# Kernel optimization log

Measured on AMD Instinct MI355X. Metric: run time of the kernel, lower is better.

Reference implementation:

```python
import jax, jax.numpy as jnp
import numpy as np

B, S, H = 32, 255, 1024
BS, WD, O = 120, 20, 10
HSZ = 2 * (BS + 1) + WD  # 262


def setup_inputs() -> dict:
    key = jax.random.key(0)
    ks = jax.random.split(key, 9)
    inv = lambda *d: 1.0 / np.sqrt(d[0])
    return {
        "state": jax.random.normal(ks[0], (B, S, H), jnp.float32),
        "head_w": jax.random.normal(ks[1], (H, BS), jnp.float32) * inv(H),
        "head_b": jax.random.normal(ks[2], (BS,), jnp.float32) * 0.02,
        "tail_w": jax.random.normal(ks[3], (H, BS), jnp.float32) * inv(H),
        "tail_b": jax.random.normal(ks[4], (BS,), jnp.float32) * 0.02,
        "U": jax.random.normal(ks[5], (O, BS, BS), jnp.float32) * inv(BS),
        "width_table": jax.random.normal(ks[6], (256, WD), jnp.float32).at[0].set(0.0),  # padding_idx=0
        "cls_w": jax.random.normal(ks[7], (O, HSZ), jnp.float32) * inv(HSZ),
        "cls_b": jax.random.normal(ks[8], (O,), jnp.float32) * 0.02,
    }


def _leaky_relu(x):
    return jnp.where(x >= 0, x, 0.01 * x)  # torch LeakyReLU default slope


def reference(state, head_w, head_b, tail_w, tail_b, U, width_table, cls_w, cls_b):
    b, s, _ = state.shape
    bs = head_w.shape[1]
    # head/tail MLPs (dropout is identity in eval)
    h = _leaky_relu(state @ head_w + head_b)  # (b, s, bs)
    t = _leaky_relu(state @ tail_w + tail_b)  # (b, s, bs)

    # bilinear term
    scores1 = jnp.einsum('bxi,oij,byj->bxyo', h, U, t)  # (b, s, s, O)

    # append bias-ones feature
    ones = jnp.ones((b, s, 1), h.dtype)
    h1 = jnp.concatenate([h, ones], axis=-1)  # (b, s, bs+1)
    t1 = jnp.concatenate([t, ones], axis=-1)

    # span-width embedding: pos[x, y] = y - x + 1, clamped to 0 for y < x
    pos = jnp.arange(s)[None, :] - jnp.arange(s)[:, None] + 1
    pos = pos * (pos > 0)
    wemb = width_table[pos]  # (s, s, WD)

    # cls(concat(h1_x, t1_y, wemb_xy)) decomposed into three small projections
    # + broadcast-add; mathematically identical to materializing affined_cat.
    Wh = cls_w[:, :bs + 1]              # (O, bs+1)
    Wt = cls_w[:, bs + 1:2 * (bs + 1)]  # (O, bs+1)
    Ww = cls_w[:, 2 * (bs + 1):]        # (O, WD)
    scores2 = (jnp.einsum('bxi,oi->bxo', h1, Wh)[:, :, None, :]
               + jnp.einsum('byi,oi->byo', t1, Wt)[:, None, :, :]
               + jnp.einsum('xyw,ow->xyo', wemb, Ww)[None]
               + cls_b)
    return scores1 + scores2
```

## Files before the change

### kernel.cpp

```cpp
#include <hip/hip_runtime.h>
#include <hip/hip_bf16.h>

using f32x4 = __attribute__((ext_vector_type(4))) float;
using s16x8 = __attribute__((ext_vector_type(8))) short;
using s16x4 = __attribute__((ext_vector_type(4))) short;

constexpr int RTOT = 32 * 255;

__device__ inline unsigned short f2bf(float x) {
    __hip_bfloat16 b = __float2bfloat16(x);
    return __builtin_bit_cast(unsigned short, b);
}
__device__ inline float bf2f(unsigned short u) {
    unsigned int t = ((unsigned int)u) << 16;
    return __builtin_bit_cast(float, t);
}
__device__ inline f32x4 mfma16(s16x8 a, s16x8 b, f32x4 c) {
    return __builtin_amdgcn_mfma_f32_16x16x32_bf16(a, b, c, 0, 0, 0);
}
__device__ inline void gload16(const unsigned short* g, unsigned short* l) {
    __builtin_amdgcn_global_load_lds(
        (const __attribute__((address_space(1))) void*)g,
        (__attribute__((address_space(3))) void*)l, 16, 0, 0);
}


__global__ __launch_bounds__(256) void convert_k(
    const float* __restrict__ head_w, const float* __restrict__ tail_w,
    const float* __restrict__ U, const float* __restrict__ wtab,
    const float* __restrict__ cls_w,
    unsigned short* __restrict__ WP, unsigned short* __restrict__ Ut,
    float* __restrict__ tblp)
{
    int gid = blockIdx.x * 256 + threadIdx.x;
    if (gid < 262144) {
        int e = gid & 7, kcp = (gid >> 3) & 7, n = (gid >> 6) & 255, ks = gid >> 14;
        int kc = kcp ^ (n & 7);
        int k = ks * 64 + kc * 8 + e;
        float v;
        if (n < 128) v = (n < 120) ? head_w[k * 120 + n] : 0.f;
        else { int nn = n - 128; v = (nn < 120) ? tail_w[k * 120 + nn] : 0.f; }
        WP[gid] = f2bf(v);
    } else if (gid < 262144 + 163840) {
        int idx = gid - 262144;
        int j = idx & 127, i2 = (idx >> 7) & 127, o = idx >> 14;
        float v = (i2 < 120 && j < 120) ? U[((size_t)o * 120 + i2) * 120 + j] : 0.f;
        Ut[(size_t)o * 16384 + (size_t)j * 128 + i2] = f2bf(v);
    } else {
        int id = gid - 262144 - 163840;
        if (id < 2560) {
            int p = id / 10, o = id - (id / 10) * 10;
            float s = 0.f;
            #pragma unroll
            for (int wq = 0; wq < 20; ++wq)
                s += wtab[p * 20 + wq] * cls_w[o * 262 + 242 + wq];
            tblp[p * 12 + o] = s;
        }
    }
}

__global__ __launch_bounds__(256) void ht_mfma(
    const float* __restrict__ state, const unsigned short* __restrict__ WP,
    const unsigned short* __restrict__ Ut,
    const float* __restrict__ head_b, const float* __restrict__ tail_b,
    const float* __restrict__ cls_w, const float* __restrict__ cls_b,
    unsigned short* __restrict__ tbuf, unsigned short* __restrict__ hUb,
    float* __restrict__ hwp, float* __restrict__ twp)
{
    __shared__ unsigned short Ss[2][32 * 64];
    __shared__ unsigned short Ws[2][256 * 64];
    const int r0 = blockIdx.x * 32;
    const int tid = threadIdx.x;
    const int w = tid >> 6, lane = tid & 63;
    const int l16 = lane & 15, kq = lane >> 4;
    const int srow = tid >> 3, skc = tid & 7;
    const float* sp = &state[(size_t)(r0 + srow) * 1024 + skc * 8];

    f32x4 acc[4][2];
    #pragma unroll
    for (int fn = 0; fn < 4; ++fn)
        #pragma unroll
        for (int fr = 0; fr < 2; ++fr) acc[fn][fr] = (f32x4){0.f, 0.f, 0.f, 0.f};

    #pragma unroll
    for (int j = 0; j < 8; ++j) {
        int off = (w * 8 + j) * 512;
        gload16(WP + off + lane * 8, &Ws[0][off]);
    }
    {
        f32x4 a0 = *(const f32x4*)sp;
        f32x4 a1 = *(const f32x4*)(sp + 4);
        s16x8 pk;
        #pragma unroll
        for (int e = 0; e < 4; ++e) { pk[e] = (short)f2bf(a0[e]); pk[e + 4] = (short)f2bf(a1[e]); }
        *(s16x8*)((char*)&Ss[0][0] + srow * 128 + ((skc * 16) ^ ((srow & 7) << 4))) = pk;
    }
    __syncthreads();

    for (int it = 0; it < 16; ++it) {
        const int cur = it & 1;
        f32x4 a0, a1;
        if (it < 15) {
            #pragma unroll
            for (int j = 0; j < 8; ++j) {
                int off = (w * 8 + j) * 512;
                gload16(WP + (it + 1) * 16384 + off + lane * 8, &Ws[cur ^ 1][off]);
            }
            a0 = *(const f32x4*)(sp + (it + 1) * 64);
            a1 = *(const f32x4*)(sp + (it + 1) * 64 + 4);
        }
        const char* SsB = (const char*)&Ss[cur][0];
        const char* WsB = (const char*)&Ws[cur][0];
        s16x8 bf[2][2];
        #pragma unroll
        for (int fr = 0; fr < 2; ++fr) {
            int rr = fr * 16 + l16;
            #pragma unroll
            for (int ks = 0; ks < 2; ++ks)
                bf[fr][ks] = *(const s16x8*)(SsB + rr * 128 + ((ks * 64 + kq * 16) ^ ((rr & 7) << 4)));
        }
        #pragma unroll
        for (int fn = 0; fn < 4; ++fn) {
            int n = w * 64 + fn * 16 + l16;
            #pragma unroll
            for (int ks = 0; ks < 2; ++ks) {
                s16x8 af = *(const s16x8*)(WsB + n * 128 + ((ks * 64 + kq * 16) ^ ((n & 7) << 4)));
                #pragma unroll
                for (int fr = 0; fr < 2; ++fr)
                    acc[fn][fr] = mfma16(af, bf[fr][ks], acc[fn][fr]);
            }
        }
        if (it < 15) {
            s16x8 pk;
            #pragma unroll
            for (int e = 0; e < 4; ++e) { pk[e] = (short)f2bf(a0[e]); pk[e + 4] = (short)f2bf(a1[e]); }
            *(s16x8*)((char*)&Ss[cur ^ 1][0] + srow * 128 + ((skc * 16) ^ ((srow & 7) << 4))) = pk;
        }
        __syncthreads();
    }

    unsigned short* Hl = &Ws[0][0];
    unsigned short* Tl = &Ws[1][0];
    #pragma unroll
    for (int fn = 0; fn < 4; ++fn) {
        const int n0 = w * 64 + fn * 16 + kq * 4;
        const int isT = n0 >= 128;
        const int c0 = n0 & 127;
        const int g = c0 >> 3, sub = c0 & 7;
        const float* bp = isT ? tail_b : head_b;
        unsigned short* dstl = isT ? Tl : Hl;
        #pragma unroll
        for (int fr = 0; fr < 2; ++fr) {
            const int rloc = fr * 16 + l16;
            const int r = r0 + rloc;
            s16x4 pk;
            #pragma unroll
            for (int e = 0; e < 4; ++e) {
                float bv = (c0 + e < 120) ? bp[c0 + e] : 0.f;
                float z = acc[fn][fr][e] + bv;
                z = (z >= 0.f) ? z : 0.01f * z;
                pk[e] = (short)f2bf(z);
            }
            *(s16x4*)&dstl[rloc * 128 + ((g ^ (rloc & 7)) << 3) + sub] = pk;
            if (isT) {
                int bq = r / 255, x = r - bq * 255;
                *(s16x4*)&tbuf[((size_t)bq * 256 + x) * 128 + ((g ^ (x & 7)) << 3) + sub] = pk;
            }
        }
    }
    __syncthreads();

    float* Wl = (float*)&Ws[0][4096];
    for (int idx = tid; idx < 2430; idx += 256) {
        if (idx < 2420) {
            int which = idx / 1210, rem = idx - which * 1210;
            int o = rem / 121, i = rem - o * 121;
            Wl[idx] = cls_w[o * 262 + which * 121 + i];
        } else Wl[idx] = cls_b[idx - 2420];
    }
    __syncthreads();

    {
        s16x8 bh[2][4];
        #pragma unroll
        for (int rf = 0; rf < 2; ++rf) {
            int rr = rf * 16 + l16;
            #pragma unroll
            for (int ks = 0; ks < 4; ++ks)
                bh[rf][ks] = *(const s16x8*)((const char*)Hl + rr * 256 +
                              ((ks * 64 + kq * 16) ^ ((rr & 7) << 4)));
        }
        size_t rbase[2]; int x4[2];
        #pragma unroll
        for (int rf = 0; rf < 2; ++rf) {
            int gr = r0 + rf * 16 + l16;
            int bq = gr / 255, x = gr - bq * 255;
            rbase[rf] = ((size_t)bq * 3072 + x * 12) * 128;
            x4[rf] = x * 4;
        }
        for (int o = 0; o < 10; ++o) {
            f32x4 acc1[2][2];
            #pragma unroll
            for (int jf = 0; jf < 2; ++jf)
                #pragma unroll
                for (int rf = 0; rf < 2; ++rf) acc1[jf][rf] = (f32x4){0.f, 0.f, 0.f, 0.f};
            #pragma unroll
            for (int ks = 0; ks < 4; ++ks) {
                #pragma unroll
                for (int jf = 0; jf < 2; ++jf) {
                    int j = w * 32 + jf * 16 + l16;
                    s16x8 af = *(const s16x8*)&Ut[(size_t)o * 16384 +
                                (size_t)j * 128 + ks * 32 + kq * 8];
                    #pragma unroll
                    for (int rf = 0; rf < 2; ++rf)
                        acc1[jf][rf] = mfma16(af, bh[rf][ks], acc1[jf][rf]);
                }
            }
            #pragma unroll
            for (int jf = 0; jf < 2; ++jf) {
                int j0 = w * 32 + jf * 16 + kq * 4;
                int g = j0 >> 3, sub = j0 & 7;
                #pragma unroll
                for (int rf = 0; rf < 2; ++rf) {
                    int key = (x4[rf] + o) & 7;
                    s16x4 pk;
                    #pragma unroll
                    for (int e = 0; e < 4; ++e) pk[e] = (short)f2bf(acc1[jf][rf][e]);
                    *(s16x4*)&hUb[rbase[rf] + (size_t)o * 128 + ((g ^ key) << 3) + sub] = pk;
                }
            }
        }
    }

    for (int d = tid; d < 640; d += 256) {
        int which = d / 320, rem = d - which * 320;
        int rr = rem / 10, o = rem - rr * 10;
        const unsigned short* row = (which ? Tl : Hl) + rr * 128;
        const float* wp2 = &Wl[which * 1210 + o * 121];
        float s = 0.f;
        #pragma unroll
        for (int c = 0; c < 15; ++c) {
            s16x8 v = *(const s16x8*)&row[(c ^ (rr & 7)) << 3];
            #pragma unroll
            for (int e = 0; e < 8; ++e)
                s += bf2f((unsigned short)v[e]) * wp2[c * 8 + e];
        }
        s += wp2[120];
        int gr = r0 + rr;
        if (!which) hwp[(size_t)gr * 12 + o] = s + Wl[2420 + o];
        else        twp[(size_t)gr * 12 + o] = s;
    }
}

__global__ __launch_bounds__(512) void main_mfma(
    const unsigned short* __restrict__ hU, const unsigned short* __restrict__ tbuf,
    const float* __restrict__ hwp, const float* __restrict__ twp,
    const float* __restrict__ tblp, float* __restrict__ out)
{
    __shared__ unsigned short Bs[256 * 128];
    __shared__ unsigned short As[2][128 * 128];
    const int wgid = blockIdx.x + (blockIdx.y << 3);
    const int virt = (wgid & 7) * 32 + (wgid >> 3);
    const int b = virt >> 3, mg = virt & 7;
    const int tid = threadIdx.x;
    const int w = tid >> 6, lane = tid & 63;
    const int l16 = lane & 15, kq = lane >> 4;
    const int wm = w >> 2, wy = w & 3;
    const size_t hUbase = (size_t)b * 3072 * 128;
    const size_t tbase = (size_t)b * 256 * 128;

    #pragma unroll
    for (int j = 0; j < 8; ++j) {
        int off = (w * 8 + j) * 512;
        gload16(&tbuf[tbase + off + lane * 8], &Bs[off]);
    }
    {
        const size_t a0 = hUbase + (size_t)(mg * 3 * 128) * 128;
        #pragma unroll
        for (int j = 0; j < 4; ++j) {
            int off = (w * 4 + j) * 512;
            gload16(&hU[a0 + off + lane * 8], &As[0][off]);
        }
    }
    __syncthreads();

    s16x8 bfr[4][4];
    #pragma unroll
    for (int ks = 0; ks < 4; ++ks)
        #pragma unroll
        for (int fy = 0; fy < 4; ++fy) {
            int row = wy * 64 + fy * 16 + l16;
            bfr[ks][fy] = *(const s16x8*)((const char*)Bs + row * 256 +
                           ((ks * 64 + kq * 16) ^ ((row & 7) << 4)));
        }

    for (int i = 0; i < 3; ++i) {
        const int m0 = (mg * 3 + i) * 128;
        if (i < 2) {
            const size_t an = hUbase + (size_t)(m0 + 128) * 128;
            #pragma unroll
            for (int j = 0; j < 4; ++j) {
                int off = (w * 4 + j) * 512;
                gload16(&hU[an + off + lane * 8], &As[(i + 1) & 1][off]);
            }
        }
        const char* AsB = (const char*)&As[i & 1][0];
        f32x4 acc[4][4];
        #pragma unroll
        for (int fm = 0; fm < 4; ++fm)
            #pragma unroll
            for (int fy = 0; fy < 4; ++fy) acc[fm][fy] = (f32x4){0.f, 0.f, 0.f, 0.f};

        #pragma unroll
        for (int ks = 0; ks < 4; ++ks) {
            s16x8 af[4];
            #pragma unroll
            for (int fm = 0; fm < 4; ++fm) {
                int row = wm * 64 + fm * 16 + l16;
                af[fm] = *(const s16x8*)(AsB + row * 256 +
                          ((ks * 64 + kq * 16) ^ ((row & 7) << 4)));
            }
            #pragma unroll
            for (int fm = 0; fm < 4; ++fm)
                #pragma unroll
                for (int fy = 0; fy < 4; ++fy)
                    acc[fm][fy] = mfma16(af[fm], bfr[ks][fy], acc[fm][fy]);
        }

        __syncthreads();

        #pragma unroll
        for (int fm = 0; fm < 4; ++fm) {
            const int ml = m0 + wm * 64 + fm * 16 + kq * 4;
            if (ml < 3060) {
                const int x = ml / 12, o0 = ml % 12;
                const int rx = b * 255 + x;
                f32x4 hv = *(const f32x4*)&hwp[(size_t)rx * 12 + o0];
                #pragma unroll
                for (int fy = 0; fy < 4; ++fy) {
                    const int y = wy * 64 + fy * 16 + l16;
                    if (y < 255) {
                        const int ry = b * 255 + y;
                        f32x4 tv = *(const f32x4*)&twp[(size_t)ry * 12 + o0];
                        int p = y - x + 1; if (p < 0) p = 0;
                        f32x4 wv = *(const f32x4*)&tblp[p * 12 + o0];
                        float* op = &out[((size_t)rx * 255 + y) * 10 + o0];
                        if (o0 < 8) {
                            float v[4];
                            #pragma unroll
                            for (int e = 0; e < 4; ++e)
                                v[e] = acc[fm][fy][e] + hv[e] + tv[e] + wv[e];
                            __builtin_memcpy(op, v, 16);
                        } else {
                            float v[2];
                            v[0] = acc[fm][fy][0] + hv[0] + tv[0] + wv[0];
                            v[1] = acc[fm][fy][1] + hv[1] + tv[1] + wv[1];
                            __builtin_memcpy(op, v, 8);
                        }
                    }
                }
            }
        }
    }
}

extern "C" void kernel_launch(void* const* d_in, const int* in_sizes, int n_in,
                              void* d_out, int out_size, void* d_ws, size_t ws_size,
                              hipStream_t stream)
{
    (void)in_sizes; (void)n_in; (void)out_size; (void)ws_size;
    const float* state  = (const float*)d_in[0];
    const float* head_w = (const float*)d_in[1];
    const float* head_b = (const float*)d_in[2];
    const float* tail_w = (const float*)d_in[3];
    const float* tail_b = (const float*)d_in[4];
    const float* U      = (const float*)d_in[5];
    const float* wtab   = (const float*)d_in[6];
    const float* cls_w  = (const float*)d_in[7];
    const float* cls_b  = (const float*)d_in[8];
    float* out = (float*)d_out;

    unsigned short* u16 = (unsigned short*)d_ws;
    unsigned short* tbuf = u16;
    unsigned short* hUb  = tbuf + 1048576;
    unsigned short* WP   = hUb + 12582912;
    unsigned short* Ut   = WP + 262144;
    float* hwp  = (float*)(Ut + 163840);
    float* twp  = hwp + 97920;
    float* tblp = twp + 97920;

    hipLaunchKernelGGL(convert_k, dim3(1674), dim3(256), 0, stream,
                       head_w, tail_w, U, wtab, cls_w, WP, Ut, tblp);
    hipLaunchKernelGGL(ht_mfma, dim3(255), dim3(256), 0, stream,
                       state, WP, Ut, head_b, tail_b, cls_w, cls_b,
                       tbuf, hUb, hwp, twp);
    hipLaunchKernelGGL(main_mfma, dim3(8, 32), dim3(512), 0, stream,
                       hUb, tbuf, hwp, twp, tblp, out);
}
```

Measured before the change: 87.05 us.

## Stage weight transpose in LDS, widen ht kernel, cache epilogue tables in LDS

The weight-pack kernel now stages head/tail weights through shared memory so global reads are coalesced and writes are 16-byte vectors, and the grid shrinks to match. The head/tail projection kernel moves to 512 threads, with each wave owning half as many output columns, to raise parallelism per block. The main kernel preloads the tail projections, width table and head projections into LDS for its epilogue, and raises wave priority around the MFMA loop. Together these aim to cut uncoalesced global traffic and latency, at the cost of more LDS use (which may lower occupancy) and larger blocks.

```diff
diff --git a/kernel.cpp b/kernel.cpp
--- a/kernel.cpp
+++ b/kernel.cpp
@@ -32,34 +32,52 @@
     unsigned short* __restrict__ WP, unsigned short* __restrict__ Ut,
     float* __restrict__ tblp)
 {
-    int gid = blockIdx.x * 256 + threadIdx.x;
-    if (gid < 262144) {
-        int e = gid & 7, kcp = (gid >> 3) & 7, n = (gid >> 6) & 255, ks = gid >> 14;
-        int kc = kcp ^ (n & 7);
-        int k = ks * 64 + kc * 8 + e;
-        float v;
-        if (n < 128) v = (n < 120) ? head_w[k * 120 + n] : 0.f;
-        else { int nn = n - 128; v = (nn < 120) ? tail_w[k * 120 + nn] : 0.f; }
-        WP[gid] = f2bf(v);
-    } else if (gid < 262144 + 163840) {
-        int idx = gid - 262144;
-        int j = idx & 127, i2 = (idx >> 7) & 127, o = idx >> 14;
-        float v = (i2 < 120 && j < 120) ? U[((size_t)o * 120 + i2) * 120 + j] : 0.f;
-        Ut[(size_t)o * 16384 + (size_t)j * 128 + i2] = f2bf(v);
+    const int tid = threadIdx.x;
+    if (blockIdx.x < 16) {
+        __shared__ unsigned short Lw[64][258];
+        const int ks = blockIdx.x;
+        for (int idx = tid; idx < 64 * 16; idx += 256) {
+            int r = idx >> 4, c = idx & 15;
+            Lw[r][120 + ((c >= 8) ? 128 : 0) + (c & 7)] = 0;
+        }
+        for (int idx = tid; idx < 7680; idx += 256) {
+            int r = idx / 120, c = idx - r * 120;
+            Lw[r][c] = f2bf(head_w[(ks * 64 + r) * 120 + c]);
+        }
+        for (int idx = tid; idx < 7680; idx += 256) {
+            int r = idx / 120, c = idx - r * 120;
+            Lw[r][128 + c] = f2bf(tail_w[(ks * 64 + r) * 120 + c]);
+        }
+        __syncthreads();
+        for (int item = tid; item < 2048; item += 256) {
+            int n = item >> 3, kcp = item & 7;
+            int kc = kcp ^ (n & 7);
+            s16x8 v;
+            #pragma unroll
+            for (int e = 0; e < 8; ++e) v[e] = (short)Lw[kc * 8 + e][n];
+            *(s16x8*)&WP[ks * 16384 + item * 8] = v;
+        }
     } else {
-        int id = gid - 262144 - 163840;
-        if (id < 2560) {
-            int p = id / 10, o = id - (id / 10) * 10;
-            float s = 0.f;
-            #pragma unroll
-            for (int wq = 0; wq < 20; ++wq)
-                s += wtab[p * 20 + wq] * cls_w[o * 262 + 242 + wq];
-            tblp[p * 12 + o] = s;
-        }
-    }
-}
-
-__global__ __launch_bounds__(256) void ht_mfma(
+        int gid = (blockIdx.x - 16) * 256 + tid;
+        if (gid < 163840) {
+            int j = gid & 127, i2 = (gid >> 7) & 127, o = gid >> 14;
+            float v = (i2 < 120 && j < 120) ? U[((size_t)o * 120 + i2) * 120 + j] : 0.f;
+            Ut[(size_t)o * 16384 + (size_t)j * 128 + i2] = f2bf(v);
+        } else {
+            int id = gid - 163840;
+            if (id < 2560) {
+                int p = id / 10, o = id - (id / 10) * 10;
+                float s = 0.f;
+                #pragma unroll
+                for (int wq = 0; wq < 20; ++wq)
+                    s += wtab[p * 20 + wq] * cls_w[o * 262 + 242 + wq];
+                tblp[p * 12 + o] = s;
+            }
+        }
+    }
+}
+
+__global__ __launch_bounds__(512) void ht_mfma(
     const float* __restrict__ state, const unsigned short* __restrict__ WP,
     const unsigned short* __restrict__ Ut,
     const float* __restrict__ head_b, const float* __restrict__ tail_b,
@@ -73,21 +91,22 @@
     const int tid = threadIdx.x;
     const int w = tid >> 6, lane = tid & 63;
     const int l16 = lane & 15, kq = lane >> 4;
-    const int srow = tid >> 3, skc = tid & 7;
+    const int srow = (tid >> 3) & 31, skc = tid & 7;
+    const bool do_s = tid < 256;
     const float* sp = &state[(size_t)(r0 + srow) * 1024 + skc * 8];
 
-    f32x4 acc[4][2];
+    f32x4 acc[2][2];
     #pragma unroll
-    for (int fn = 0; fn < 4; ++fn)
+    for (int fn = 0; fn < 2; ++fn)
         #pragma unroll
         for (int fr = 0; fr < 2; ++fr) acc[fn][fr] = (f32x4){0.f, 0.f, 0.f, 0.f};
 
     #pragma unroll
-    for (int j = 0; j < 8; ++j) {
-        int off = (w * 8 + j) * 512;
+    for (int j = 0; j < 4; ++j) {
+        int off = (w * 4 + j) * 512;
         gload16(WP + off + lane * 8, &Ws[0][off]);
     }
-    {
+    if (do_s) {
         f32x4 a0 = *(const f32x4*)sp;
         f32x4 a1 = *(const f32x4*)(sp + 4);
         s16x8 pk;
@@ -102,12 +121,14 @@
         f32x4 a0, a1;
         if (it < 15) {
             #pragma unroll
-            for (int j = 0; j < 8; ++j) {
-                int off = (w * 8 + j) * 512;
+            for (int j = 0; j < 4; ++j) {
+                int off = (w * 4 + j) * 512;
                 gload16(WP + (it + 1) * 16384 + off + lane * 8, &Ws[cur ^ 1][off]);
             }
-            a0 = *(const f32x4*)(sp + (it + 1) * 64);
-            a1 = *(const f32x4*)(sp + (it + 1) * 64 + 4);
+            if (do_s) {
+                a0 = *(const f32x4*)(sp + (it + 1) * 64);
+                a1 = *(const f32x4*)(sp + (it + 1) * 64 + 4);
+            }
         }
         const char* SsB = (const char*)&Ss[cur][0];
         const char* WsB = (const char*)&Ws[cur][0];
@@ -120,8 +141,8 @@
                 bf[fr][ks] = *(const s16x8*)(SsB + rr * 128 + ((ks * 64 + kq * 16) ^ ((rr & 7) << 4)));
         }
         #pragma unroll
-        for (int fn = 0; fn < 4; ++fn) {
-            int n = w * 64 + fn * 16 + l16;
+        for (int fn = 0; fn < 2; ++fn) {
+            int n = w * 32 + fn * 16 + l16;
             #pragma unroll
             for (int ks = 0; ks < 2; ++ks) {
                 s16x8 af = *(const s16x8*)(WsB + n * 128 + ((ks * 64 + kq * 16) ^ ((n & 7) << 4)));
@@ -130,7 +151,7 @@
                     acc[fn][fr] = mfma16(af, bf[fr][ks], acc[fn][fr]);
             }
         }
-        if (it < 15) {
+        if (it < 15 && do_s) {
             s16x8 pk;
             #pragma unroll
             for (int e = 0; e < 4; ++e) { pk[e] = (short)f2bf(a0[e]); pk[e + 4] = (short)f2bf(a1[e]); }
@@ -142,8 +163,8 @@
     unsigned short* Hl = &Ws[0][0];
     unsigned short* Tl = &Ws[1][0];
     #pragma unroll
-    for (int fn = 0; fn < 4; ++fn) {
-        const int n0 = w * 64 + fn * 16 + kq * 4;
+    for (int fn = 0; fn < 2; ++fn) {
+        const int n0 = w * 32 + fn * 16 + kq * 4;
         const int isT = n0 >= 128;
         const int c0 = n0 & 127;
         const int g = c0 >> 3, sub = c0 & 7;
@@ -171,7 +192,7 @@
     __syncthreads();
 
     float* Wl = (float*)&Ws[0][4096];
-    for (int idx = tid; idx < 2430; idx += 256) {
+    for (int idx = tid; idx < 2430; idx += 512) {
         if (idx < 2420) {
             int which = idx / 1210, rem = idx - which * 1210;
             int o = rem / 121, i = rem - o * 121;
@@ -198,41 +219,33 @@
             rbase[rf] = ((size_t)bq * 3072 + x * 12) * 128;
             x4[rf] = x * 4;
         }
+        const int j = w * 16 + l16;
+        const int j0 = w * 16 + kq * 4;
+        const int g2 = j0 >> 3, sub2 = j0 & 7;
         for (int o = 0; o < 10; ++o) {
-            f32x4 acc1[2][2];
-            #pragma unroll
-            for (int jf = 0; jf < 2; ++jf)
-                #pragma unroll
-                for (int rf = 0; rf < 2; ++rf) acc1[jf][rf] = (f32x4){0.f, 0.f, 0.f, 0.f};
+            f32x4 acc1[2];
+            #pragma unroll
+            for (int rf = 0; rf < 2; ++rf) acc1[rf] = (f32x4){0.f, 0.f, 0.f, 0.f};
             #pragma unroll
             for (int ks = 0; ks < 4; ++ks) {
-                #pragma unroll
-                for (int jf = 0; jf < 2; ++jf) {
-                    int j = w * 32 + jf * 16 + l16;
-                    s16x8 af = *(const s16x8*)&Ut[(size_t)o * 16384 +
-                                (size_t)j * 128 + ks * 32 + kq * 8];
-                    #pragma unroll
-                    for (int rf = 0; rf < 2; ++rf)
-                        acc1[jf][rf] = mfma16(af, bh[rf][ks], acc1[jf][rf]);
-                }
-            }
-            #pragma unroll
-            for (int jf = 0; jf < 2; ++jf) {
-                int j0 = w * 32 + jf * 16 + kq * 4;
-                int g = j0 >> 3, sub = j0 & 7;
-                #pragma unroll
-                for (int rf = 0; rf < 2; ++rf) {
-                    int key = (x4[rf] + o) & 7;
-                    s16x4 pk;
-                    #pragma unroll
-                    for (int e = 0; e < 4; ++e) pk[e] = (short)f2bf(acc1[jf][rf][e]);
-                    *(s16x4*)&hUb[rbase[rf] + (size_t)o * 128 + ((g ^ key) << 3) + sub] = pk;
-                }
-            }
-        }
-    }
-
-    for (int d = tid; d < 640; d += 256) {
+                s16x8 af = *(const s16x8*)&Ut[(size_t)o * 16384 +
+                            (size_t)j * 128 + ks * 32 + kq * 8];
+                #pragma unroll
+                for (int rf = 0; rf < 2; ++rf)
+                    acc1[rf] = mfma16(af, bh[rf][ks], acc1[rf]);
+            }
+            #pragma unroll
+            for (int rf = 0; rf < 2; ++rf) {
+                int key = (x4[rf] + o) & 7;
+                s16x4 pk;
+                #pragma unroll
+                for (int e = 0; e < 4; ++e) pk[e] = (short)f2bf(acc1[rf][e]);
+                *(s16x4*)&hUb[rbase[rf] + (size_t)o * 128 + ((g2 ^ key) << 3) + sub2] = pk;
+            }
+        }
+    }
+
+    for (int d = tid; d < 640; d += 512) {
         int which = d / 320, rem = d - which * 320;
         int rr = rem / 10, o = rem - rr * 10;
         const unsigned short* row = (which ? Tl : Hl) + rr * 128;
@@ -259,6 +272,9 @@
 {
     __shared__ unsigned short Bs[256 * 128];
     __shared__ unsigned short As[2][128 * 128];
+    __shared__ float Ts[3060];
+    __shared__ float Tb[3072];
+    __shared__ float Hw[384];
     const int wgid = blockIdx.x + (blockIdx.y << 3);
     const int virt = (wgid & 7) * 32 + (wgid >> 3);
     const int b = virt >> 3, mg = virt & 7;
@@ -282,6 +298,13 @@
             gload16(&hU[a0 + off + lane * 8], &As[0][off]);
         }
     }
+    {
+        const float* twb = twp + (size_t)b * 3060;
+        for (int idx = tid; idx < 3060; idx += 512) Ts[idx] = twb[idx];
+        for (int idx = tid; idx < 3072; idx += 512) Tb[idx] = tblp[idx];
+        if (tid < 384 && mg * 384 + tid < 3060)
+            Hw[tid] = hwp[(size_t)b * 3060 + mg * 384 + tid];
+    }
     __syncthreads();
 
     s16x8 bfr[4][4];
@@ -311,6 +334,7 @@
             #pragma unroll
             for (int fy = 0; fy < 4; ++fy) acc[fm][fy] = (f32x4){0.f, 0.f, 0.f, 0.f};
 
+        __builtin_amdgcn_s_setprio(1);
         #pragma unroll
         for (int ks = 0; ks < 4; ++ks) {
             s16x8 af[4];
@@ -326,6 +350,7 @@
                 for (int fy = 0; fy < 4; ++fy)
                     acc[fm][fy] = mfma16(af[fm], bfr[ks][fy], acc[fm][fy]);
         }
+        __builtin_amdgcn_s_setprio(0);
 
         __syncthreads();
 
@@ -335,15 +360,14 @@
             if (ml < 3060) {
                 const int x = ml / 12, o0 = ml % 12;
                 const int rx = b * 255 + x;
-                f32x4 hv = *(const f32x4*)&hwp[(size_t)rx * 12 + o0];
+                f32x4 hv = *(const f32x4*)&Hw[(x - mg * 32) * 12 + o0];
                 #pragma unroll
                 for (int fy = 0; fy < 4; ++fy) {
                     const int y = wy * 64 + fy * 16 + l16;
                     if (y < 255) {
-                        const int ry = b * 255 + y;
-                        f32x4 tv = *(const f32x4*)&twp[(size_t)ry * 12 + o0];
+                        f32x4 tv = *(const f32x4*)&Ts[y * 12 + o0];
                         int p = y - x + 1; if (p < 0) p = 0;
-                        f32x4 wv = *(const f32x4*)&tblp[p * 12 + o0];
+                        f32x4 wv = *(const f32x4*)&Tb[p * 12 + o0];
                         float* op = &out[((size_t)rx * 255 + y) * 10 + o0];
                         if (o0 < 8) {
                             float v[4];
@@ -389,9 +413,9 @@
     float* twp  = hwp + 97920;
     float* tblp = twp + 97920;
 
-    hipLaunchKernelGGL(convert_k, dim3(1674), dim3(256), 0, stream,
+    hipLaunchKernelGGL(convert_k, dim3(666), dim3(256), 0, stream,
                        head_w, tail_w, U, wtab, cls_w, WP, Ut, tblp);
-    hipLaunchKernelGGL(ht_mfma, dim3(255), dim3(256), 0, stream,
+    hipLaunchKernelGGL(ht_mfma, dim3(255), dim3(512), 0, stream,
                        state, WP, Ut, head_b, tail_b, cls_w, cls_b,
                        tbuf, hUb, hwp, twp);
     hipLaunchKernelGGL(main_mfma, dim3(8, 32), dim3(512), 0, stream,
```

Measured after the change: 79.85 us. 1.09x faster.
